# Kernel optimization log

Hardware: AMD Instinct MI355X
Metric: run time of the kernel (lower is better)

## Reference

```python
import jax, jax.numpy as jnp
import numpy as np

B, N, C_IN = 16, 4096, 64
NPOINT = 1024
RADII = (0.2, 0.4)
NSAMPLES = (32, 64)
MLPS = ((64, 64, 128), (64, 64, 128))
C_TOTAL = sum(m[-1] for m in MLPS)


def setup_inputs() -> dict:
    key = jax.random.key(0)
    ks = jax.random.split(key, 24)
    inp = {
        "xyz": jax.random.uniform(ks[0], (B, N, 3), jnp.float32),
        "features": jax.random.normal(ks[1], (B, N, C_IN), jnp.float32),
        "w_att": jax.random.normal(ks[2], (3 * NPOINT, C_TOTAL), jnp.float32) * 0.02,
        "b_att": jnp.zeros((C_TOTAL,), jnp.float32),
    }
    k = 3
    for g, mlp in enumerate(MLPS):
        cin = 3 + C_IN
        for l, cout in enumerate(mlp):
            inp[f"w{g}_{l}"] = jax.random.normal(ks[k], (cout, cin), jnp.float32) * (1.0 / np.sqrt(cin))
            inp[f"b{g}_{l}"] = jnp.zeros((cout,), jnp.float32)
            k += 1
            cin = cout
    return inp


def _fps(xyz, npoint):
    # furthest point sampling; xyz (B,N,3) -> idx (B,npoint) int32. First idx is 0 (matches CUDA op).
    b, n, _ = xyz.shape
    init_idx = jnp.zeros((b,), jnp.int32)
    init_dist = jnp.full((b, n), 1e10, xyz.dtype)

    def body(carry, _):
        dists, last = carry
        last_pt = jnp.take_along_axis(xyz, last[:, None, None].astype(jnp.int32), axis=1)  # (B,1,3)
        d = jnp.sum((xyz - last_pt) ** 2, axis=-1)  # (B,N)
        dists = jnp.minimum(dists, d)
        nxt = jnp.argmax(dists, axis=-1).astype(jnp.int32)
        return (dists, nxt), nxt

    (_, _), rest = jax.lax.scan(body, (init_dist, init_idx), None, length=npoint - 1)
    return jnp.concatenate([init_idx[None, :], rest], axis=0).T  # (B, npoint)


def _ball_query(radius, nsample, xyz, new_xyz):
    # first-nsample points of xyz within radius of each new_xyz center (slots padded with first hit)
    n = xyz.shape[1]
    d2 = jnp.sum((new_xyz[:, :, None, :] - xyz[:, None, :, :]) ** 2, axis=-1)  # (B,S,N)
    mask = d2 < radius * radius
    order_key = jnp.where(mask, jnp.arange(n, dtype=jnp.int32)[None, None, :], n)
    idx = jnp.argsort(order_key, axis=-1)[..., :nsample].astype(jnp.int32)  # (B,S,nsample)
    valid = jnp.take_along_axis(mask, idx, axis=-1)
    return jnp.where(valid, idx, idx[..., :1])


def _group(xyz, new_xyz, features, idx):
    # -> (B, 3+C, S, nsample): relative xyz concat grouped features
    b, s, ns = idx.shape
    flat = idx.reshape(b, s * ns)
    gx = jnp.take_along_axis(xyz, flat[..., None], axis=1).reshape(b, s, ns, 3)
    gx = gx - new_xyz[:, :, None, :]
    gf = jnp.take_along_axis(features, flat[..., None], axis=1).reshape(b, s, ns, features.shape[-1])
    return jnp.transpose(jnp.concatenate([gx, gf], axis=-1), (0, 3, 1, 2))


def reference(xyz, features, w_att, b_att,
              w0_0, b0_0, w0_1, b0_1, w0_2, b0_2,
              w1_0, b1_0, w1_1, b1_1, w1_2, b1_2):
    xyz_sg = jax.lax.stop_gradient(xyz)  # index selection is non-differentiable (matches CUDA ops)
    fps_idx = _fps(xyz_sg, NPOINT)  # (B, npoint)
    new_xyz = jnp.take_along_axis(xyz, fps_idx[..., None], axis=1)  # (B, npoint, 3)

    # attention gate from sampled coordinates: (B, 3, npoint) flattened -> (B, C_TOTAL)
    att_in = jnp.transpose(new_xyz, (0, 2, 1)).reshape(xyz.shape[0], 3 * NPOINT)
    att = jax.nn.sigmoid(att_in @ w_att + b_att)  # (B, C_TOTAL)

    layer_sets = (((w0_0, b0_0), (w0_1, b0_1), (w0_2, b0_2)),
                  ((w1_0, b1_0), (w1_1, b1_1), (w1_2, b1_2)))
    pooled = []
    new_xyz_sg = jax.lax.stop_gradient(new_xyz)
    for radius, ns, layers in zip(RADII, NSAMPLES, layer_sets):
        idx = _ball_query(radius, ns, xyz_sg, new_xyz_sg)
        x = _group(xyz, new_xyz, features, idx)  # (B, 3+C, S, ns)
        for w, b in layers:  # shared 1x1 conv + ReLU per layer
            x = jax.nn.relu(jnp.einsum('oc,bcsn->bosn', w, x) + b[None, :, None, None])
        pooled.append(jnp.max(x, axis=-1))  # max over nsample -> (B, cout, S)

    features_cat = jnp.concatenate(pooled, axis=1)  # (B, C_TOTAL, S)
    features_end = features_cat * att[:, :, None]
    return new_xyz, features_end
```

## Files before the change

kernel.cpp:

```cpp
#include <hip/hip_runtime.h>
#include <cstdint>
#include <cstddef>


constexpr int B_ = 16, N_ = 4096, S_ = 1024;
constexpr int WT_G = 67*64 + 64*64 + 128*64 + 64 + 64 + 128;
constexpr int FPS_T = 512;
constexpr int WT_BLK = (2*WT_G + FPS_T - 1) / FPS_T;
constexpr int G1_BLK = 2 * B_ * (N_ / 256);

constexpr int WS_XYZF = 0;
constexpr int WS_NXYZ = B_*N_*4;
constexpr int WS_ATT  = WS_NXYZ + B_*S_*3;
constexpr int WS_WT   = WS_ATT + B_*256;
constexpr int WS_IDX0 = WS_WT + 2*WT_G;
constexpr int WS_IDX1 = WS_IDX0 + B_*S_*32;
constexpr int WS_F1   = WS_IDX1 + B_*S_*64;

__global__ __launch_bounds__(256) void g1_kernel(
    const float* __restrict__ xyz, const float* __restrict__ feats,
    const float* __restrict__ w00, const float* __restrict__ w10,
    float* __restrict__ f1) {
  __shared__ float wfs[67 * 64];
  const int fid = blockIdx.x;
  const int g = fid >> 8, b = (fid >> 4) & 15, chunk = fid & 15;
  const float* w = g ? w10 : w00;
  for (int k = threadIdx.x; k < 67*64; k += 256) {
    int c = k >> 6, o = k & 63;
    wfs[k] = w[o*67 + c];
  }
  __syncthreads();
  const int p = chunk * 256 + threadIdx.x;
  const float* xr = xyz + ((size_t)b * N_ + p) * 3;
  const float* fr = feats + ((size_t)b * N_ + p) * 64;
  float acc[64];
  {
    float x0 = xr[0], x1 = xr[1], x2 = xr[2];
#pragma unroll
    for (int j = 0; j < 64; j += 4) {
      float4 wA = *(const float4*)&wfs[0*64 + j];
      acc[j+0] = wA.x * x0; acc[j+1] = wA.y * x0;
      acc[j+2] = wA.z * x0; acc[j+3] = wA.w * x0;
    }
#pragma unroll
    for (int j = 0; j < 64; j += 4) {
      float4 wA = *(const float4*)&wfs[1*64 + j];
      acc[j+0] = fmaf(wA.x, x1, acc[j+0]); acc[j+1] = fmaf(wA.y, x1, acc[j+1]);
      acc[j+2] = fmaf(wA.z, x1, acc[j+2]); acc[j+3] = fmaf(wA.w, x1, acc[j+3]);
    }
#pragma unroll
    for (int j = 0; j < 64; j += 4) {
      float4 wA = *(const float4*)&wfs[2*64 + j];
      acc[j+0] = fmaf(wA.x, x2, acc[j+0]); acc[j+1] = fmaf(wA.y, x2, acc[j+1]);
      acc[j+2] = fmaf(wA.z, x2, acc[j+2]); acc[j+3] = fmaf(wA.w, x2, acc[j+3]);
    }
  }
  for (int c = 0; c < 64; ++c) {
    float v = fr[c];
    const float* wr = &wfs[(3 + c) * 64];
#pragma unroll
    for (int j = 0; j < 64; j += 4) {
      float4 w4 = *(const float4*)&wr[j];
      acc[j+0] = fmaf(w4.x, v, acc[j+0]); acc[j+1] = fmaf(w4.y, v, acc[j+1]);
      acc[j+2] = fmaf(w4.z, v, acc[j+2]); acc[j+3] = fmaf(w4.w, v, acc[j+3]);
    }
  }
  float* op = f1 + (((size_t)g * B_ + b) * N_ + p) * 64;
#pragma unroll
  for (int j = 0; j < 64; j += 4) {
    float4 r = make_float4(acc[j], acc[j+1], acc[j+2], acc[j+3]);
    *(float4*)&op[j] = r;
  }
}

__global__ __launch_bounds__(512) void fps_wt_kernel(
    const float* __restrict__ xyz,
    const float* __restrict__ w00, const float* __restrict__ w01,
    const float* __restrict__ w02, const float* __restrict__ b00,
    const float* __restrict__ b01, const float* __restrict__ b02,
    const float* __restrict__ w10, const float* __restrict__ w11,
    const float* __restrict__ w12, const float* __restrict__ b10,
    const float* __restrict__ b11, const float* __restrict__ b12,
    float4* __restrict__ xyzf, float* __restrict__ wt,
    float* __restrict__ nxyz, float* __restrict__ out_nxyz) {
  constexpr int PPT = 8;
  __shared__ float sx[N_*3];
  __shared__ int   selidx[S_];
  __shared__ alignas(16) unsigned long long redP[2][8];
  __shared__ alignas(16) float4 redC[2][8];

  if (blockIdx.x >= B_) {
    int wid = (blockIdx.x - B_) * FPS_T + threadIdx.x;
    if (wid >= 2*WT_G) return;
    int g = wid / WT_G, r = wid % WT_G;
    float val;
    if (r < 4288) {
      int c = r >> 6, o = r & 63;
      val = (g ? w10 : w00)[o*67 + c];
    } else if (r < 8384) {
      int rr = r - 4288; int c = rr >> 6, o = rr & 63;
      val = (g ? w11 : w01)[o*64 + c];
    } else if (r < 16576) {
      int rr = r - 8384; int c = rr >> 7, o = rr & 127;
      val = (g ? w12 : w02)[o*64 + c];
    } else {
      int rr = r - 16576;
      val = (rr < 64)  ? (g ? b10 : b00)[rr]
          : (rr < 128) ? (g ? b11 : b01)[rr - 64]
                       : (g ? b12 : b02)[rr - 128];
    }
    wt[g*WT_G + r] = val;
    return;
  }

  const int b = blockIdx.x, t = threadIdx.x;
  const int wv = t >> 6;
  const float* xr = xyz + (size_t)b * N_ * 3;
  for (int k = t; k < N_*3; k += FPS_T) sx[k] = xr[k];
  if (t == 0) selidx[0] = 0;
  __syncthreads();
  float px[PPT], py[PPT], pz[PPT], m[PPT];
#pragma unroll
  for (int p = 0; p < PPT; ++p) {
    int idx = t * PPT + p;
    px[p] = sx[idx*3+0]; py[p] = sx[idx*3+1]; pz[p] = sx[idx*3+2];
    m[p] = 1e10f;
  }
  float lx = sx[0], ly = sx[1], lz = sx[2];
  for (int i = 1; i < S_; ++i) {
#pragma unroll
    for (int p = 0; p < PPT; ++p) {
      float dx = __fsub_rn(px[p], lx), dy = __fsub_rn(py[p], ly), dz = __fsub_rn(pz[p], lz);
      float d = __fadd_rn(__fadd_rn(__fmul_rn(dx,dx), __fmul_rn(dy,dy)), __fmul_rn(dz,dz));
      m[p] = fminf(m[p], d);
    }
    float h0 = fmaxf(fmaxf(m[0], m[1]), fmaxf(m[2], m[3]));
    float h1 = fmaxf(fmaxf(m[4], m[5]), fmaxf(m[6], m[7]));
    float bv = fmaxf(h0, h1);
    int bp = PPT - 1;
#pragma unroll
    for (int p = PPT - 2; p >= 0; --p)
      if (m[p] == bv) bp = p;
    const int bi = t * PPT + bp;
    unsigned vm = __float_as_uint(bv);
#define DPP_MAX(ctrl) { unsigned o = (unsigned)__builtin_amdgcn_update_dpp((int)vm, (int)vm, (ctrl), 0xf, 0xf, false); vm = vm > o ? vm : o; }
    DPP_MAX(0x111)
    DPP_MAX(0x112)
    DPP_MAX(0x114)
    DPP_MAX(0x118)
    DPP_MAX(0x142)
    DPP_MAX(0x143)
#undef DPP_MAX
    const unsigned wmaxu = (unsigned)__builtin_amdgcn_readlane((int)vm, 63);
    const unsigned long long mk = __ballot(__float_as_uint(bv) == wmaxu);
    const int fl = (int)__builtin_ctzll(mk);
    const int widx = __builtin_amdgcn_readlane(bi, fl);
    const int par = i & 1;
    if (t == (widx >> 3)) {
      const int psel = widx & 7;
      float gx = px[0], gy = py[0], gz = pz[0];
#pragma unroll
      for (int p = 1; p < PPT; ++p)
        if (psel == p) { gx = px[p]; gy = py[p]; gz = pz[p]; }
      redP[par][wv] = ((unsigned long long)wmaxu << 32) | (unsigned)(~widx);
      redC[par][wv] = make_float4(gx, gy, gz, 0.f);
    }
    __syncthreads();
    ulonglong2 pA = *(const ulonglong2*)&redP[par][0];
    ulonglong2 pB = *(const ulonglong2*)&redP[par][2];
    ulonglong2 pC = *(const ulonglong2*)&redP[par][4];
    ulonglong2 pD = *(const ulonglong2*)&redP[par][6];
    unsigned long long q0 = pA.x > pA.y ? pA.x : pA.y;
    unsigned long long q1 = pB.x > pB.y ? pB.x : pB.y;
    unsigned long long q2 = pC.x > pC.y ? pC.x : pC.y;
    unsigned long long q3 = pD.x > pD.y ? pD.x : pD.y;
    unsigned long long r0 = q0 > q1 ? q0 : q1;
    unsigned long long r1 = q2 > q3 ? q2 : q3;
    unsigned long long win = r0 > r1 ? r0 : r1;
    const int fi = (int)(~(unsigned)win);
    const int ws = fi >> 9;
    float4 fc = redC[par][ws];
    lx = fc.x; ly = fc.y; lz = fc.z;
    if (t == 0) selidx[i] = fi;
  }
  __syncthreads();
  for (int k = t; k < S_; k += FPS_T) {
    int id = selidx[k];
    float x = sx[id*3], y = sx[id*3+1], z = sx[id*3+2];
    int o = (b * S_ + k) * 3;
    nxyz[o] = x; nxyz[o+1] = y; nxyz[o+2] = z;
    out_nxyz[o] = x; out_nxyz[o+1] = y; out_nxyz[o+2] = z;
  }
  for (int k = t; k < N_; k += FPS_T) {
    float4 v; v.x = sx[k*3]; v.y = sx[k*3+1]; v.z = sx[k*3+2]; v.w = 0.f;
    xyzf[b * N_ + k] = v;
  }
}

__global__ __launch_bounds__(256) void ballq_att_kernel(
    const float4* __restrict__ xyzf, const float* __restrict__ nxyz,
    int* __restrict__ idx0buf, int* __restrict__ idx1buf,
    const float* __restrict__ w_att, const float* __restrict__ b_att,
    float* __restrict__ att) {
  __shared__ float ai[3 * S_];
  if (blockIdx.x >= B_*S_/4) {
    int b = blockIdx.x - B_*S_/4, t = threadIdx.x;
    for (int k = t; k < 3 * S_; k += 256) {
      int d = k >> 10, s = k & 1023;
      ai[k] = nxyz[(b * S_ + s) * 3 + d];
    }
    __syncthreads();
    float acc = b_att[t];
#pragma unroll 8
    for (int k = 0; k < 3 * S_; ++k)
      acc = fmaf(ai[k], w_att[k * 256 + t], acc);
    att[b * 256 + t] = 1.f / (1.f + expf(-acc));
    return;
  }
  const float r2a = (float)(0.2 * 0.2), r2b = (float)(0.4 * 0.4);
  int lane = threadIdx.x & 63;
  int cid = blockIdx.x * 4 + (threadIdx.x >> 6);
  int b = cid >> 10;
  float cx = nxyz[cid*3], cy = nxyz[cid*3+1], cz = nxyz[cid*3+2];
  const float4* xb = xyzf + b * N_;
  int cnt0 = 0, cnt1 = 0, first0 = 0, first1 = 0;
  const unsigned long long below = (1ull << lane) - 1ull;
  for (int base = 0; base < N_; base += 64) {
    float4 P = xb[base + lane];
    float dx = __fsub_rn(cx, P.x), dy = __fsub_rn(cy, P.y), dz = __fsub_rn(cz, P.z);
    float d2 = __fadd_rn(__fadd_rn(__fmul_rn(dx,dx), __fmul_rn(dy,dy)), __fmul_rn(dz,dz));
    bool h0 = d2 < r2a, h1 = d2 < r2b;
    unsigned long long m0 = __ballot(h0), m1 = __ballot(h1);
    if (cnt0 == 0 && m0 != 0ull) first0 = base + (int)__builtin_ctzll(m0);
    if (cnt1 == 0 && m1 != 0ull) first1 = base + (int)__builtin_ctzll(m1);
    if (h0) {
      int pos = cnt0 + (int)__popcll(m0 & below);
      if (pos < 32) idx0buf[cid * 32 + pos] = base + lane;
    }
    if (h1) {
      int pos = cnt1 + (int)__popcll(m1 & below);
      if (pos < 64) idx1buf[cid * 64 + pos] = base + lane;
    }
    cnt0 += (int)__popcll(m0);
    cnt1 += (int)__popcll(m1);
    if (cnt0 >= 32 && cnt1 >= 64) break;
  }
  if (cnt0 < 32)
    for (int p = cnt0 + lane; p < 32; p += 64) idx0buf[cid * 32 + p] = first0;
  if (cnt1 < 64)
    for (int p = cnt1 + lane; p < 64; p += 64) idx1buf[cid * 64 + p] = first1;
}

template<int NS>
__device__ __forceinline__ void mlp_body(int bi, float* xs, int* pidx,
    float* c1s, const float* __restrict__ f1g,
    const float* __restrict__ nxyz, const float* __restrict__ att,
    const int* __restrict__ idxbuf, const float* __restrict__ wt,
    float* __restrict__ outf, int g) {
  constexpr int NCEN = 128 / NS;
  constexpr int XS = 132;
  float* red = xs;
  const int t = threadIdx.x;
  const int cid0 = bi * NCEN;
  const int b = cid0 >> 10;

  const float* w0  = wt;
  const float* w1  = wt + 67*64;
  const float* w2  = w1 + 64*64;
  const float* bb0 = w2 + 64*128;
  const float* bb1 = bb0 + 64;
  const float* bb2 = bb1 + 64;

  if (t < 128) {
    const int col = t;
    const int cidg = cid0 + col / NS;
    pidx[col] = idxbuf[cidg * NS + (col % NS)];
  }
  if (t < 64 * NCEN) {
    const int o = t & 63, ci = t >> 6;
    const int cid = cid0 + ci;
    float nx = nxyz[cid*3], ny = nxyz[cid*3+1], nz = nxyz[cid*3+2];
    c1s[ci*64 + o] = fmaf(w0[128+o], nz, fmaf(w0[64+o], ny, w0[o]*nx));
  }
  __syncthreads();

  const int og = t & 15, cg = t >> 4;
  float acc[4][8];

  {
    float4 bv = *(const float4*)&bb0[og*4];
    const int ctr = (cg * 8) / NS;
    float4 cv = *(const float4*)&c1s[ctr*64 + og*4];
    float bc[4] = {bv.x - cv.x, bv.y - cv.y, bv.z - cv.z, bv.w - cv.w};
    const int4 pA = *(const int4*)&pidx[cg*8];
    const int4 pB = *(const int4*)&pidx[cg*8 + 4];
    int pc[8] = {pA.x, pA.y, pA.z, pA.w, pB.x, pB.y, pB.z, pB.w};
#pragma unroll
    for (int cc = 0; cc < 8; ++cc) {
      float4 fv = *(const float4*)&f1g[((size_t)b * N_ + pc[cc]) * 64 + og*4];
      acc[0][cc] = bc[0] + fv.x;
      acc[1][cc] = bc[1] + fv.y;
      acc[2][cc] = bc[2] + fv.z;
      acc[3][cc] = bc[3] + fv.w;
    }
  }
#pragma unroll
  for (int oo = 0; oo < 4; ++oo) {
    float4 y0, y1;
    y0.x=fmaxf(acc[oo][0],0.f); y0.y=fmaxf(acc[oo][1],0.f);
    y0.z=fmaxf(acc[oo][2],0.f); y0.w=fmaxf(acc[oo][3],0.f);
    y1.x=fmaxf(acc[oo][4],0.f); y1.y=fmaxf(acc[oo][5],0.f);
    y1.z=fmaxf(acc[oo][6],0.f); y1.w=fmaxf(acc[oo][7],0.f);
    *(float4*)&xs[(og*4+oo)*XS + cg*8]     = y0;
    *(float4*)&xs[(og*4+oo)*XS + cg*8 + 4] = y1;
  }
  __syncthreads();

  {
    float4 bv = *(const float4*)&bb1[og*4];
    float b4[4] = {bv.x, bv.y, bv.z, bv.w};
#pragma unroll
    for (int oo = 0; oo < 4; ++oo)
#pragma unroll
      for (int cc = 0; cc < 8; ++cc) acc[oo][cc] = b4[oo];
    for (int k = 0; k < 64; ++k) {
      float4 x0 = *(const float4*)&xs[k*XS + cg*8];
      float4 x1 = *(const float4*)&xs[k*XS + cg*8 + 4];
      float4 wv = *(const float4*)&w1[k*64 + og*4];
      float x8[8] = {x0.x,x0.y,x0.z,x0.w,x1.x,x1.y,x1.z,x1.w};
      float w4[4] = {wv.x,wv.y,wv.z,wv.w};
#pragma unroll
      for (int oo = 0; oo < 4; ++oo)
#pragma unroll
        for (int cc = 0; cc < 8; ++cc) acc[oo][cc] = fmaf(w4[oo], x8[cc], acc[oo][cc]);
    }
  }
  __syncthreads();
#pragma unroll
  for (int oo = 0; oo < 4; ++oo) {
    float4 y0, y1;
    y0.x=fmaxf(acc[oo][0],0.f); y0.y=fmaxf(acc[oo][1],0.f);
    y0.z=fmaxf(acc[oo][2],0.f); y0.w=fmaxf(acc[oo][3],0.f);
    y1.x=fmaxf(acc[oo][4],0.f); y1.y=fmaxf(acc[oo][5],0.f);
    y1.z=fmaxf(acc[oo][6],0.f); y1.w=fmaxf(acc[oo][7],0.f);
    *(float4*)&xs[(og*4+oo)*XS + cg*8]     = y0;
    *(float4*)&xs[(og*4+oo)*XS + cg*8 + 4] = y1;
  }
  __syncthreads();

  float acc3[8][8];
  {
    float4 b0v = *(const float4*)&bb2[og*8];
    float4 b1v = *(const float4*)&bb2[og*8 + 4];
    float b8[8] = {b0v.x,b0v.y,b0v.z,b0v.w,b1v.x,b1v.y,b1v.z,b1v.w};
#pragma unroll
    for (int oo = 0; oo < 8; ++oo)
#pragma unroll
      for (int cc = 0; cc < 8; ++cc) acc3[oo][cc] = b8[oo];
    for (int k = 0; k < 64; ++k) {
      float4 x0 = *(const float4*)&xs[k*XS + cg*8];
      float4 x1 = *(const float4*)&xs[k*XS + cg*8 + 4];
      float4 wa = *(const float4*)&w2[k*128 + og*8];
      float4 wb = *(const float4*)&w2[k*128 + og*8 + 4];
      float x8[8] = {x0.x,x0.y,x0.z,x0.w,x1.x,x1.y,x1.z,x1.w};
      float w8[8] = {wa.x,wa.y,wa.z,wa.w,wb.x,wb.y,wb.z,wb.w};
#pragma unroll
      for (int oo = 0; oo < 8; ++oo)
#pragma unroll
        for (int cc = 0; cc < 8; ++cc) acc3[oo][cc] = fmaf(w8[oo], x8[cc], acc3[oo][cc]);
    }
  }
  float pm[8];
#pragma unroll
  for (int oo = 0; oo < 8; ++oo) {
    float v = fmaxf(acc3[oo][0], 0.f);
#pragma unroll
    for (int cc = 1; cc < 8; ++cc) v = fmaxf(v, fmaxf(acc3[oo][cc], 0.f));
    pm[oo] = v;
  }
#pragma unroll
  for (int oo = 0; oo < 8; ++oo) {
    pm[oo] = fmaxf(pm[oo], __shfl_xor(pm[oo], 16));
    pm[oo] = fmaxf(pm[oo], __shfl_xor(pm[oo], 32));
  }
  __syncthreads();
  if ((t & 63) < 16) {
    int w = t >> 6;
#pragma unroll
    for (int oo = 0; oo < 8; ++oo) red[w*128 + og*8 + oo] = pm[oo];
  }
  __syncthreads();

  const int ch = t & 127;
  const float a = att[b*256 + g*128 + ch];
  if (NS == 64) {
    int c = t >> 7;
    float v = fmaxf(red[(2*c)*128 + ch], red[(2*c+1)*128 + ch]);
    int s = (cid0 + c) & 1023;
    outf[((size_t)(b*256 + g*128 + ch)) * 1024 + s] = v * a;
  } else {
#pragma unroll
    for (int kk = 0; kk < 2; ++kk) {
      int c = (t >> 7) * 2 + kk;
      float v = red[c*128 + ch];
      int s = (cid0 + c) & 1023;
      outf[((size_t)(b*256 + g*128 + ch)) * 1024 + s] = v * a;
    }
  }
}

__global__ __launch_bounds__(256, 4) void mlp_kernel(
    const float* __restrict__ f1, const float* __restrict__ nxyz,
    const float* __restrict__ att, const int* __restrict__ idx0,
    const int* __restrict__ idx1, const float* __restrict__ wt,
    float* __restrict__ outf) {
  constexpr int XS = 132;
  __shared__ float xs[64 * XS];
  __shared__ int pidx[128];
  __shared__ float c1s[256];
  if (blockIdx.x < 4096)
    mlp_body<32>(blockIdx.x, xs, pidx, c1s, f1, nxyz, att, idx0, wt, outf, 0);
  else
    mlp_body<64>(blockIdx.x - 4096, xs, pidx, c1s, f1 + (size_t)B_*N_*64,
                 nxyz, att, idx1, wt + WT_G, outf, 1);
}

extern "C" void kernel_launch(void* const* d_in, const int* in_sizes, int n_in,
                              void* d_out, int out_size, void* d_ws, size_t ws_size,
                              hipStream_t stream) {
  const float* xyz   = (const float*)d_in[0];
  const float* feats = (const float*)d_in[1];
  const float* w_att = (const float*)d_in[2];
  const float* b_att = (const float*)d_in[3];
  const float* w00 = (const float*)d_in[4];
  const float* b00 = (const float*)d_in[5];
  const float* w01 = (const float*)d_in[6];
  const float* b01 = (const float*)d_in[7];
  const float* w02 = (const float*)d_in[8];
  const float* b02 = (const float*)d_in[9];
  const float* w10 = (const float*)d_in[10];
  const float* b10 = (const float*)d_in[11];
  const float* w11 = (const float*)d_in[12];
  const float* b11 = (const float*)d_in[13];
  const float* w12 = (const float*)d_in[14];
  const float* b12 = (const float*)d_in[15];

  float* wsf = (float*)d_ws;
  int*   wsi = (int*)d_ws;
  float4* xyzf = (float4*)(wsf + WS_XYZF);
  float* nxyz  = wsf + WS_NXYZ;
  float* att   = wsf + WS_ATT;
  float* wt    = wsf + WS_WT;
  int* idx0 = wsi + WS_IDX0;
  int* idx1 = wsi + WS_IDX1;
  float* f1 = wsf + WS_F1;

  float* out  = (float*)d_out;
  float* outf = out + B_ * S_ * 3;

  hipLaunchKernelGGL(g1_kernel, dim3(G1_BLK), dim3(256), 0, stream,
                     xyz, feats, w00, w10, f1);
  hipLaunchKernelGGL(fps_wt_kernel, dim3(B_ + WT_BLK), dim3(FPS_T), 0, stream,
                     xyz, w00, w01, w02, b00, b01, b02, w10, w11, w12,
                     b10, b11, b12, xyzf, wt, nxyz, out);
  hipLaunchKernelGGL(ballq_att_kernel, dim3(B_*S_/4 + B_), dim3(256), 0, stream,
                     xyzf, nxyz, idx0, idx1, w_att, b_att, att);
  hipLaunchKernelGGL(mlp_kernel, dim3(12288), dim3(256), 0, stream,
                     f1, nxyz, att, idx0, idx1, wt, outf);
}
```

Baseline: 1.480 ms.

## Double FPS block threads and reduce cross-wave argmax with DPP and readlane

The furthest-point-sampling block now uses 1024 threads with 4 points each instead of 512 threads with 8, halving the per-thread serial work in each of the 1023 iterations. The cross-wave reduction drops the packed 64-bit key scan and instead loads 16 per-wave candidates into lanes, reduces them with DPP max and a ballot, and broadcasts index and coordinates with readlane. The price is more waves meeting at each per-iteration barrier and a longer DPP chain for the second reduction stage. The weight-transpose blocks also change size because they share FPS_T.

```diff
diff --git a/kernel.cpp b/kernel.cpp
--- a/kernel.cpp
+++ b/kernel.cpp
@@ -5,7 +5,7 @@
 
 constexpr int B_ = 16, N_ = 4096, S_ = 1024;
 constexpr int WT_G = 67*64 + 64*64 + 128*64 + 64 + 64 + 128;
-constexpr int FPS_T = 512;
+constexpr int FPS_T = 1024;
 constexpr int WT_BLK = (2*WT_G + FPS_T - 1) / FPS_T;
 constexpr int G1_BLK = 2 * B_ * (N_ / 256);
 
@@ -73,7 +73,7 @@
   }
 }
 
-__global__ __launch_bounds__(512) void fps_wt_kernel(
+__global__ __launch_bounds__(1024) void fps_wt_kernel(
     const float* __restrict__ xyz,
     const float* __restrict__ w00, const float* __restrict__ w01,
     const float* __restrict__ w02, const float* __restrict__ b00,
@@ -83,11 +83,13 @@
     const float* __restrict__ b11, const float* __restrict__ b12,
     float4* __restrict__ xyzf, float* __restrict__ wt,
     float* __restrict__ nxyz, float* __restrict__ out_nxyz) {
-  constexpr int PPT = 8;
+  constexpr int PPT = 4;
+  constexpr int NW  = 16;
   __shared__ float sx[N_*3];
   __shared__ int   selidx[S_];
-  __shared__ alignas(16) unsigned long long redP[2][8];
-  __shared__ alignas(16) float4 redC[2][8];
+  __shared__ unsigned redV[2][NW];
+  __shared__ int      redI[2][NW];
+  __shared__ alignas(16) float4 redC[2][NW];
 
   if (blockIdx.x >= B_) {
     int wid = (blockIdx.x - B_) * FPS_T + threadIdx.x;
@@ -115,6 +117,7 @@
 
   const int b = blockIdx.x, t = threadIdx.x;
   const int wv = t >> 6;
+  const int lane = t & 63;
   const float* xr = xyz + (size_t)b * N_ * 3;
   for (int k = t; k < N_*3; k += FPS_T) sx[k] = xr[k];
   if (t == 0) selidx[0] = 0;
@@ -127,6 +130,15 @@
     m[p] = 1e10f;
   }
   float lx = sx[0], ly = sx[1], lz = sx[2];
+
+#define DPP_MAX(v) \
+  { unsigned o_ = (unsigned)__builtin_amdgcn_update_dpp((int)(v), (int)(v), 0x111, 0xf, 0xf, false); (v) = (v) > o_ ? (v) : o_; \
+    o_ = (unsigned)__builtin_amdgcn_update_dpp((int)(v), (int)(v), 0x112, 0xf, 0xf, false); (v) = (v) > o_ ? (v) : o_; \
+    o_ = (unsigned)__builtin_amdgcn_update_dpp((int)(v), (int)(v), 0x114, 0xf, 0xf, false); (v) = (v) > o_ ? (v) : o_; \
+    o_ = (unsigned)__builtin_amdgcn_update_dpp((int)(v), (int)(v), 0x118, 0xf, 0xf, false); (v) = (v) > o_ ? (v) : o_; \
+    o_ = (unsigned)__builtin_amdgcn_update_dpp((int)(v), (int)(v), 0x142, 0xf, 0xf, false); (v) = (v) > o_ ? (v) : o_; \
+    o_ = (unsigned)__builtin_amdgcn_update_dpp((int)(v), (int)(v), 0x143, 0xf, 0xf, false); (v) = (v) > o_ ? (v) : o_; }
+
   for (int i = 1; i < S_; ++i) {
 #pragma unroll
     for (int p = 0; p < PPT; ++p) {
@@ -134,55 +146,47 @@
       float d = __fadd_rn(__fadd_rn(__fmul_rn(dx,dx), __fmul_rn(dy,dy)), __fmul_rn(dz,dz));
       m[p] = fminf(m[p], d);
     }
-    float h0 = fmaxf(fmaxf(m[0], m[1]), fmaxf(m[2], m[3]));
-    float h1 = fmaxf(fmaxf(m[4], m[5]), fmaxf(m[6], m[7]));
-    float bv = fmaxf(h0, h1);
+    float bv = fmaxf(fmaxf(m[0], m[1]), fmaxf(m[2], m[3]));
     int bp = PPT - 1;
 #pragma unroll
     for (int p = PPT - 2; p >= 0; --p)
       if (m[p] == bv) bp = p;
     const int bi = t * PPT + bp;
     unsigned vm = __float_as_uint(bv);
-#define DPP_MAX(ctrl) { unsigned o = (unsigned)__builtin_amdgcn_update_dpp((int)vm, (int)vm, (ctrl), 0xf, 0xf, false); vm = vm > o ? vm : o; }
-    DPP_MAX(0x111)
-    DPP_MAX(0x112)
-    DPP_MAX(0x114)
-    DPP_MAX(0x118)
-    DPP_MAX(0x142)
-    DPP_MAX(0x143)
-#undef DPP_MAX
+    DPP_MAX(vm)
     const unsigned wmaxu = (unsigned)__builtin_amdgcn_readlane((int)vm, 63);
     const unsigned long long mk = __ballot(__float_as_uint(bv) == wmaxu);
     const int fl = (int)__builtin_ctzll(mk);
     const int widx = __builtin_amdgcn_readlane(bi, fl);
     const int par = i & 1;
-    if (t == (widx >> 3)) {
-      const int psel = widx & 7;
+    if (t == (widx >> 2)) {
+      const int psel = widx & 3;
       float gx = px[0], gy = py[0], gz = pz[0];
 #pragma unroll
       for (int p = 1; p < PPT; ++p)
         if (psel == p) { gx = px[p]; gy = py[p]; gz = pz[p]; }
-      redP[par][wv] = ((unsigned long long)wmaxu << 32) | (unsigned)(~widx);
+      redV[par][wv] = wmaxu;
+      redI[par][wv] = widx;
       redC[par][wv] = make_float4(gx, gy, gz, 0.f);
     }
     __syncthreads();
-    ulonglong2 pA = *(const ulonglong2*)&redP[par][0];
-    ulonglong2 pB = *(const ulonglong2*)&redP[par][2];
-    ulonglong2 pC = *(const ulonglong2*)&redP[par][4];
-    ulonglong2 pD = *(const ulonglong2*)&redP[par][6];
-    unsigned long long q0 = pA.x > pA.y ? pA.x : pA.y;
-    unsigned long long q1 = pB.x > pB.y ? pB.x : pB.y;
-    unsigned long long q2 = pC.x > pC.y ? pC.x : pC.y;
-    unsigned long long q3 = pD.x > pD.y ? pD.x : pD.y;
-    unsigned long long r0 = q0 > q1 ? q0 : q1;
-    unsigned long long r1 = q2 > q3 ? q2 : q3;
-    unsigned long long win = r0 > r1 ? r0 : r1;
-    const int fi = (int)(~(unsigned)win);
-    const int ws = fi >> 9;
-    float4 fc = redC[par][ws];
-    lx = fc.x; ly = fc.y; lz = fc.z;
+    const int cl = lane & (NW - 1);
+    unsigned rv = redV[par][cl];
+    int      ri = redI[par][cl];
+    float4   rc = redC[par][cl];
+    unsigned cand = (lane < NW) ? rv : 0u;
+    unsigned cm = cand;
+    DPP_MAX(cm)
+    const unsigned bmax = (unsigned)__builtin_amdgcn_readlane((int)cm, 63);
+    const unsigned long long mk2 = __ballot((lane < NW) && (cand == bmax));
+    const int wstar = (int)__builtin_ctzll(mk2);
+    const int fi = __builtin_amdgcn_readlane(ri, wstar);
+    lx = __uint_as_float((unsigned)__builtin_amdgcn_readlane(__float_as_int(rc.x), wstar));
+    ly = __uint_as_float((unsigned)__builtin_amdgcn_readlane(__float_as_int(rc.y), wstar));
+    lz = __uint_as_float((unsigned)__builtin_amdgcn_readlane(__float_as_int(rc.z), wstar));
     if (t == 0) selidx[i] = fi;
   }
+#undef DPP_MAX
   __syncthreads();
   for (int k = t; k < S_; k += FPS_T) {
     int id = selidx[k];
```

Result: slower. 1.633 ms (+10.3%).
